# Performance work log

Measured on AMD Instinct MI355X. Metric: run time of the kernel, lower is better.

## Reference

```python
import jax, jax.numpy as jnp
import numpy as np

L, H, E, FF, MAXP, NKNOW = 4, 8, 512, 2048, 10, 1000
B, S = 4, 128
HD = E // H


def _layer_norm(x, g, b, eps=1e-5):
    m = x.mean(-1, keepdims=True)
    v = ((x - m) ** 2).mean(-1, keepdims=True)
    return (x - m) / jnp.sqrt(v + eps) * g + b


def setup_inputs() -> dict:
    key = jax.random.key(0)
    ks = jax.random.split(key, 16)
    x = jax.random.normal(ks[0], (B, S, E), jnp.float32)
    adj = jax.random.randint(ks[1], (B, S, S), 0, 2, jnp.int32)
    s_mask = jax.random.randint(ks[2], (B, S, S), 0, 2, jnp.int32)
    o_mask = jax.random.randint(ks[3], (B, S, S), 0, 2, jnp.int32)
    knowledge = jax.random.normal(ks[4], (NKNOW, E), jnp.float32)
    know_adj = jax.random.randint(ks[5], (B, S, S), 0, NKNOW, jnp.int64)
    pos_mask = jax.random.randint(ks[6], (S, S), 0, MAXP + 1, jnp.int32)
    # relative position embedding tables (padding_idx=0 -> row 0 zero)
    pe_k = jax.random.normal(ks[7], (MAXP + 1, HD), jnp.float32).at[0].set(0.0)
    pe_v = jax.random.normal(ks[8], (MAXP + 1, HD), jnp.float32).at[0].set(0.0)
    sc = 0.02
    # stacked per-layer parameters
    Wq = jax.random.normal(ks[9], (L, E, E), jnp.float32) * sc
    Wk = jax.random.normal(ks[10], (L, E, E), jnp.float32) * sc
    Wvs = jax.random.normal(ks[11], (L, E, E), jnp.float32) * sc
    Wvo = jax.random.normal(ks[12], (L, E, E), jnp.float32) * sc
    Wo = jax.random.normal(ks[13], (L, E, E), jnp.float32) * sc
    Wkn = jax.random.normal(ks[14], (L, E, E), jnp.float32) * sc
    kf = jax.random.split(ks[15], 4)
    w1 = jax.random.normal(kf[0], (L, FF, E), jnp.float32) * sc
    b1 = jnp.zeros((L, FF), jnp.float32)
    w2 = jax.random.normal(kf[1], (L, E, FF), jnp.float32) * sc
    b2 = jnp.zeros((L, E), jnp.float32)
    ln1_g = jnp.ones((L, E), jnp.float32)
    ln1_b = jnp.zeros((L, E), jnp.float32)
    ln2_g = jnp.ones((L, E), jnp.float32)
    ln2_b = jnp.zeros((L, E), jnp.float32)
    return dict(x=x, adj=adj, s_mask=s_mask, o_mask=o_mask, knowledge=knowledge,
                know_adj=know_adj, pos_mask=pos_mask, pe_k=pe_k, pe_v=pe_v,
                Wq=Wq, Wk=Wk, Wvs=Wvs, Wvo=Wvo, Wo=Wo, Wkn=Wkn,
                ln1_g=ln1_g, ln1_b=ln1_b, w1=w1, b1=b1, w2=w2, b2=b2,
                ln2_g=ln2_g, ln2_b=ln2_b)


def reference(x, adj, s_mask, o_mask, knowledge, know_adj, pos_mask, pe_k, pe_v,
              Wq, Wk, Wvs, Wvo, Wo, Wkn, ln1_g, ln1_b, w1, b1, w2, b2,
              ln2_g, ln2_b):
    bsz, slen, emb = x.shape
    hd = emb // H
    scaling = float(hd) ** (-0.5)
    # relative position embeddings, shared across batch/heads: [S,S,hd]
    pos = jnp.clip(pos_mask, 0, MAXP)
    rel_k = pe_k[pos]
    rel_v = pe_v[pos]
    adj_f = adj.astype(x.dtype)[:, None, :, :]          # [B,1,S,S]
    sm = s_mask.astype(x.dtype)[:, None, :, :, None]    # [B,1,S,S,1]
    om = o_mask.astype(x.dtype)[:, None, :, :, None]
    know_feat = knowledge[know_adj]                      # [B,S,S,E]

    def split_heads(t):  # [B,S,E] -> [B,H,S,hd]
        return t.reshape(bsz, slen, H, hd).transpose(0, 2, 1, 3)

    h = x
    for i in range(L):
        q = split_heads(h @ Wq[i].T)
        k = split_heads(h @ Wk[i].T)
        vs = split_heads(h @ Wvs[i].T)
        vo = split_heads(h @ Wvo[i].T)
        # knowledge projection -> [B,H,S,S,hd]
        know = (know_feat @ Wkn[i].T).reshape(bsz, slen, slen, H, hd).transpose(0, 3, 1, 2, 4)
        # multiplicative attention: q_i * (k_j + know_ij + rel_ij) summed over hd
        rel = (know + rel_k[None, None]) + k[:, :, None, :, :]
        scores = jnp.einsum('bhid,bhijd->bhij', q, rel) * scaling
        scores = scores - (1.0 - adj_f) * 1e30          # mask_logic
        attn = jax.nn.softmax(scores, axis=-1)           # [B,H,S,S]
        value = vs[:, :, None, :, :] * sm + vo[:, :, None, :, :] * om  # [B,H,S,S,hd]
        attn_sum = jnp.einsum('bhijd,bhij->bhid', value + rel_v[None, None], attn)
        out = attn_sum.transpose(0, 2, 1, 3).reshape(bsz, slen, emb) @ Wo[i].T
        h = _layer_norm(h + out, ln1_g[i], ln1_b[i])
        ff = jax.nn.relu(h @ w1[i].T + b1[i]) @ w2[i].T + b2[i]
        h = _layer_norm(h + ff, ln2_g[i], ln2_b[i])
    return h
```

## Files before the change

kernel.cpp:

```cpp
#include <hip/hip_runtime.h>

#define EE 512
#define SS 128
#define BB 4
#define NH 8
#define HD 64
#define FFD 2048
#define NL 4
#define LDQ 2048

typedef short bf16x8 __attribute__((ext_vector_type(8)));
typedef float f32x4 __attribute__((ext_vector_type(4)));

__device__ __forceinline__ ushort f2bf(float f) {
    uint u = __float_as_uint(f);
    return (ushort)((u + 0x7fffu + ((u >> 16) & 1u)) >> 16);
}
__device__ __forceinline__ float bflo(uint u) { return __uint_as_float(u << 16); }
__device__ __forceinline__ float bfhi(uint u) { return __uint_as_float(u & 0xffff0000u); }

__device__ __forceinline__ void gll16(const ushort* g, ushort* l) {
    __builtin_amdgcn_global_load_lds(
        (const __attribute__((address_space(1))) void*)g,
        (__attribute__((address_space(3))) void*)l, 16, 0, 0);
}

struct GemmJob {
    const ushort* A; const ushort* B;
    float* Cf; ushort* Cb;
    const float* bias; const float* resid;
    int M, N, K, flags, nbx, base;
};

__global__ __launch_bounds__(256) void gemm_bf16(GemmJob j0, GemmJob j1, int njobs)
{
    __shared__ ushort As[3][2048];
    __shared__ ushort Bs[3][4096];
    GemmJob j = (njobs > 1 && (int)blockIdx.x >= j1.base) ? j1 : j0;
    const int bid = (int)blockIdx.x - j.base;
    const int by = bid / j.nbx, bx = bid % j.nbx;
    const int rowBase = by * 32, colBase = bx * 64;
    const int t = threadIdx.x, lane = t & 63, wid = t >> 6;
    const int wc = wid;
    const int Kd = j.K, Md = j.M, Nd = j.N;

    const ushort* Bg = j.B + (size_t)(colBase + lane) * Kd;
    int gr = rowBase + (lane & 31); if (gr >= Md) gr = Md - 1;
    const ushort* Ag = j.A + (size_t)gr * Kd + (2 * wid + (lane >> 5)) * 8;

    f32x4 acc[2];
#pragma unroll
    for (int m = 0; m < 2; ++m)
#pragma unroll
        for (int r = 0; r < 4; ++r) acc[m][r] = 0.f;

    auto STAGE = [&](int bf, int tt) {
        const int k0 = tt << 6;
        gll16(Bg + k0 + (2 * wid) * 8,     &Bs[bf][(2 * wid) * 512]);
        gll16(Bg + k0 + (2 * wid + 1) * 8, &Bs[bf][(2 * wid + 1) * 512]);
        gll16(Ag + k0,                     &As[bf][(2 * wid) * 256]);
    };
    auto COMPUTE = [&](int bf) {
#pragma unroll
        for (int kc = 0; kc < 2; ++kc) {
            const int c16 = kc * 4 + (lane >> 4);
            bf16x8 af[2], bfg;
#pragma unroll
            for (int m = 0; m < 2; ++m) {
                const int row = m * 16 + (lane & 15);
                af[m] = *(const bf16x8*)&As[bf][c16 * 256 + row * 8];
            }
            {
                const int rowb = wc * 16 + (lane & 15);
                bfg = *(const bf16x8*)&Bs[bf][c16 * 512 + rowb * 8];
            }
#pragma unroll
            for (int m = 0; m < 2; ++m)
                acc[m] = __builtin_amdgcn_mfma_f32_16x16x32_bf16(af[m], bfg, acc[m], 0, 0, 0);
        }
    };

    const int nt = Kd >> 6;
    STAGE(0, 0);
    STAGE(1, 1);
    asm volatile("s_waitcnt vmcnt(3)" ::: "memory");
    __builtin_amdgcn_s_barrier();
    int bc = 0, bs = 2;
    for (int tt = 0; tt < nt; ++tt) {
        const bool more = (tt + 2) < nt;
        if (more) STAGE(bs, tt + 2);
        COMPUTE(bc);
        if (tt < nt - 1) {
            if (more) asm volatile("s_waitcnt vmcnt(3)" ::: "memory");
            else      asm volatile("s_waitcnt vmcnt(0)" ::: "memory");
            __builtin_amdgcn_s_barrier();
        }
        bc = bc == 2 ? 0 : bc + 1;
        bs = bs == 2 ? 0 : bs + 1;
    }

    const int cl = lane & 15, rh = lane >> 4;
#pragma unroll
    for (int m = 0; m < 2; ++m) {
        const int col = colBase + wc * 16 + cl;
        const int row0 = rowBase + m * 16 + rh * 4;
#pragma unroll
        for (int r = 0; r < 4; ++r) {
            const int rr = row0 + r;
            if (rr < Md) {
                float v = acc[m][r];
                if (j.flags & 1) v += j.bias[col];
                if (j.flags & 2) v = fmaxf(v, 0.f);
                if (j.resid) v += j.resid[(size_t)rr * Nd + col];
                if (j.Cf) j.Cf[(size_t)rr * Nd + col] = v;
                if (j.Cb) j.Cb[(size_t)rr * Nd + col] = f2bf(v);
            }
        }
    }
}

__global__ __launch_bounds__(256) void score_gemm(
    const ushort* __restrict__ qkvv, const ushort* __restrict__ kprojl,
    float* __restrict__ qk, float* __restrict__ qkk)
{
    __shared__ ushort As[2048];
    __shared__ ushort Bs[4096];
    const int t = threadIdx.x, lane = t & 63, wid = t >> 6;
    const int bid = blockIdx.x;
    const ushort *Abase, *Bbase;
    float* Cbase; int crs, rowBase, colBase;
    if (bid < 256) {
        const int q = bid >> 3, sub = bid & 7;
        const int b = q >> 3, h = q & 7;
        rowBase = (sub >> 1) * 32; colBase = (sub & 1) * 64;
        Abase = qkvv + (size_t)(b * SS) * LDQ + h * HD;
        Bbase = qkvv + (size_t)(b * SS) * LDQ + 512 + h * HD;
        Cbase = qk + (size_t)b * 131072 + h * 128;
        crs = 1024;
    } else {
        const int idx = bid - 256;
        const int h = idx >> 8, sub = idx & 255;
        rowBase = (sub >> 4) * 32; colBase = (sub & 15) * 64;
        Abase = qkvv + h * HD;
        Bbase = kprojl + h * HD;
        Cbase = qkk + (size_t)h * 1024;
        crs = 8192;
    }
    {
        const ushort* Bg = Bbase + (size_t)(colBase + lane) * LDQ;
        const ushort* Ag = Abase + (size_t)(rowBase + (lane & 31)) * LDQ
                           + (2 * wid + (lane >> 5)) * 8;
        gll16(Bg + (2 * wid) * 8,     &Bs[(2 * wid) * 512]);
        gll16(Bg + (2 * wid + 1) * 8, &Bs[(2 * wid + 1) * 512]);
        gll16(Ag,                     &As[(2 * wid) * 256]);
        asm volatile("s_waitcnt vmcnt(0)" ::: "memory");
        __builtin_amdgcn_s_barrier();
    }
    f32x4 acc[2];
#pragma unroll
    for (int m = 0; m < 2; ++m)
#pragma unroll
        for (int r = 0; r < 4; ++r) acc[m][r] = 0.f;
#pragma unroll
    for (int kc = 0; kc < 2; ++kc) {
        const int c16 = kc * 4 + (lane >> 4);
        bf16x8 af[2], bfg;
#pragma unroll
        for (int m = 0; m < 2; ++m) {
            const int row = m * 16 + (lane & 15);
            af[m] = *(const bf16x8*)&As[c16 * 256 + row * 8];
        }
        {
            const int rowb = wid * 16 + (lane & 15);
            bfg = *(const bf16x8*)&Bs[c16 * 512 + rowb * 8];
        }
#pragma unroll
        for (int m = 0; m < 2; ++m)
            acc[m] = __builtin_amdgcn_mfma_f32_16x16x32_bf16(af[m], bfg, acc[m], 0, 0, 0);
    }
    const int cl = lane & 15, rh = lane >> 4;
#pragma unroll
    for (int m = 0; m < 2; ++m) {
        const int col = colBase + wid * 16 + cl;
        const int row0 = rowBase + m * 16 + rh * 4;
#pragma unroll
        for (int r = 0; r < 4; ++r)
            Cbase[(size_t)(row0 + r) * crs + col] = acc[m][r];
    }
}

struct PrepArgs {
    const float *Wq, *Wk, *Wvs, *Wvo, *Wo, *Wkn, *w1, *w2, *know, *x, *pek;
    ushort *wqkvv, *wo, *wkn, *w1b, *w2b, *knowb, *hb, *kpe;
    float *h;
};
#define P4_WQKVV 1048576
#define P4_B1 (P4_WQKVV + 262144)
#define P4_B2 (P4_B1 + 262144)
#define P4_B3 (P4_B2 + 1048576)
#define P4_B4 (P4_B3 + 1048576)
#define P4_B5 (P4_B4 + 128000)
#define P4_B6 (P4_B5 + 65536)
#define P4_TOT (P4_B6 + 5632)

__global__ __launch_bounds__(256) void prep_kernel(PrepArgs pa)
{
    const int i = blockIdx.x * 256 + threadIdx.x;
    if (i >= P4_TOT) return;
    const float4* src;
    ushort4* dst;
    if (i < P4_WQKVV) {
        const int l = i >> 18, r = i & 262143, q = r >> 16;
        const float* s = (q == 0 ? pa.Wq : q == 1 ? pa.Wk : q == 2 ? pa.Wvs : pa.Wvo);
        src = (const float4*)s + l * 65536 + (r & 65535);
        dst = (ushort4*)pa.wqkvv + i;
    } else if (i < P4_B1) {
        const int k = i - P4_WQKVV;
        src = (const float4*)pa.Wo + k; dst = (ushort4*)pa.wo + k;
    } else if (i < P4_B2) {
        const int k = i - P4_B1;
        src = (const float4*)pa.Wkn + k; dst = (ushort4*)pa.wkn + k;
    } else if (i < P4_B3) {
        const int k = i - P4_B2;
        src = (const float4*)pa.w1 + k; dst = (ushort4*)pa.w1b + k;
    } else if (i < P4_B4) {
        const int k = i - P4_B3;
        src = (const float4*)pa.w2 + k; dst = (ushort4*)pa.w2b + k;
    } else if (i < P4_B5) {
        const int k = i - P4_B4;
        src = (const float4*)pa.know + k; dst = (ushort4*)pa.knowb + k;
    } else if (i < P4_B6) {
        const int k = i - P4_B5;
        src = (const float4*)pa.x + k; dst = (ushort4*)pa.hb + k;
        ((float4*)pa.h)[k] = *src;
    } else {
        const int k = i - P4_B6;
        const int c4 = k * 4;
        const int p = c4 >> 11, col = c4 & 2047, d = col & 63;
        src = (const float4*)(pa.pek + p * 64 + d);
        dst = (ushort4*)(pa.kpe + (size_t)(1000 + p) * 2048 + col);
    }
    float4 v = *src;
    ushort4 o; o.x = f2bf(v.x); o.y = f2bf(v.y); o.z = f2bf(v.z); o.w = f2bf(v.w);
    *dst = o;
}

__global__ __launch_bounds__(256) void ln_kernel(
    const float* __restrict__ X, const float* __restrict__ g,
    const float* __restrict__ bt, float* __restrict__ Yf,
    ushort* __restrict__ Yb, int rows)
{
    const int w = threadIdx.x >> 6, lane = threadIdx.x & 63;
    const int row = blockIdx.x * 4 + w;
    if (row >= rows) return;
    const float* x = X + (size_t)row * EE;
    float4 v0 = ((const float4*)x)[lane];
    float4 v1 = ((const float4*)x)[lane + 64];
    float s  = v0.x + v0.y + v0.z + v0.w + v1.x + v1.y + v1.z + v1.w;
    float q2 = v0.x*v0.x + v0.y*v0.y + v0.z*v0.z + v0.w*v0.w
             + v1.x*v1.x + v1.y*v1.y + v1.z*v1.z + v1.w*v1.w;
#pragma unroll
    for (int o = 32; o; o >>= 1) { s += __shfl_xor(s, o); q2 += __shfl_xor(q2, o); }
    const float mean = s * (1.f / EE);
    const float var  = q2 * (1.f / EE) - mean * mean;
    const float rstd = rsqrtf(var + 1e-5f);
    float4 g0 = ((const float4*)g)[lane],  g1 = ((const float4*)g)[lane + 64];
    float4 b0 = ((const float4*)bt)[lane], b1 = ((const float4*)bt)[lane + 64];
    float4 o0, o1;
    o0.x = (v0.x - mean) * rstd * g0.x + b0.x;
    o0.y = (v0.y - mean) * rstd * g0.y + b0.y;
    o0.z = (v0.z - mean) * rstd * g0.z + b0.z;
    o0.w = (v0.w - mean) * rstd * g0.w + b0.w;
    o1.x = (v1.x - mean) * rstd * g1.x + b1.x;
    o1.y = (v1.y - mean) * rstd * g1.y + b1.y;
    o1.z = (v1.z - mean) * rstd * g1.z + b1.z;
    o1.w = (v1.w - mean) * rstd * g1.w + b1.w;
    float* y = Yf + (size_t)row * EE;
    ((float4*)y)[lane] = o0;
    ((float4*)y)[lane + 64] = o1;
    ushort* yb = Yb + (size_t)row * EE;
    ushort4 p0, p1;
    p0.x = f2bf(o0.x); p0.y = f2bf(o0.y); p0.z = f2bf(o0.z); p0.w = f2bf(o0.w);
    p1.x = f2bf(o1.x); p1.y = f2bf(o1.y); p1.z = f2bf(o1.z); p1.w = f2bf(o1.w);
    ((ushort4*)yb)[lane] = p0;
    ((ushort4*)yb)[lane + 64] = p1;
}

__global__ __launch_bounds__(256) void attn_kernel(
    const ushort* __restrict__ qkvv, const float* __restrict__ qk,
    const float* __restrict__ qkk,
    const int* __restrict__ know_adj, const int* __restrict__ pos_mask,
    const float* __restrict__ pe_v,
    const int* __restrict__ adj, const int* __restrict__ s_mask,
    const int* __restrict__ o_mask, ushort* __restrict__ asum)
{
    const int blk = blockIdx.x;
    const int b = blk >> 7, i = blk & 127;
    const int t = threadIdx.x;

    __shared__ float sc[NH][SS];
    __shared__ float ap[NH][11];
    __shared__ float ws_s[SS], wo_s[SS], amask_s[SS];
    __shared__ int   pos_s[SS], n_s[SS];

    const float* qkrow  = qk + (size_t)b * 131072 + (size_t)i * 1024;
    const float* qkkrow = qkk + (size_t)(b * SS + i) * 8192;

    if (t < 128) {
        const int jj = t;
        const size_t off = ((size_t)(b * SS + i)) * SS + jj;
        n_s[jj]     = know_adj[off];
        amask_s[jj] = adj[off] ? 0.f : 1e30f;
        ws_s[jj]    = (float)s_mask[off];
        wo_s[jj]    = (float)o_mask[off];
        int p = pos_mask[i * SS + jj];
        pos_s[jj] = p > 10 ? 10 : (p < 0 ? 0 : p);
        if (t < 88) ap[t / 11][t % 11] = 0.f;
    } else {
        const int tt = t - 128;
        ((float4*)&sc[0][0])[tt]       = ((const float4*)qkrow)[tt];
        ((float4*)&sc[0][0])[tt + 128] = ((const float4*)qkrow)[tt + 128];
    }
    __syncthreads();

    {
        const int h = t >> 5, j0 = (t & 31) * 4;
        const float* qh = qkkrow + h * 1024;
#pragma unroll
        for (int u = 0; u < 4; ++u) {
            const int jj = j0 + u;
            const float v = sc[h][jj] + qh[n_s[jj]] + qh[1000 + pos_s[jj]];
            sc[h][jj] = v * 0.125f - amask_s[jj];
        }
    }
    __syncthreads();

    {
        const int w = t >> 6, lane = t & 63;
#pragma unroll
        for (int hh = 0; hh < 2; ++hh) {
            const int h = w * 2 + hh;
            float v0 = sc[h][lane], v1 = sc[h][lane + 64];
            float m = fmaxf(v0, v1);
#pragma unroll
            for (int o = 32; o; o >>= 1) m = fmaxf(m, __shfl_xor(m, o));
            float e0 = __expf(v0 - m), e1 = __expf(v1 - m);
            float ssum = e0 + e1;
#pragma unroll
            for (int o = 32; o; o >>= 1) ssum += __shfl_xor(ssum, o);
            const float inv = 1.f / ssum;
            e0 *= inv; e1 *= inv;
            sc[h][lane] = e0; sc[h][lane + 64] = e1;
            atomicAdd(&ap[h][pos_s[lane]], e0);
            atomicAdd(&ap[h][pos_s[lane + 64]], e1);
        }
    }
    __syncthreads();

    {
        const int h = t >> 5, d0 = (t & 31) * 2;
        float a0 = 0.f, a1 = 0.f;
        const ushort* vbase = qkvv + (size_t)b * SS * LDQ + 1024 + h * HD + d0;
        for (int j0 = 0; j0 < SS; j0 += 8) {
            uint vsp[8], vop[8];
#pragma unroll
            for (int u = 0; u < 8; ++u) {
                const ushort* r = vbase + (size_t)(j0 + u) * LDQ;
                vsp[u] = *(const uint*)r;
                vop[u] = *(const uint*)(r + 512);
            }
#pragma unroll
            for (int u = 0; u < 8; ++u) {
                const int jj = j0 + u;
                const float aw = sc[h][jj];
                const float wsj = ws_s[jj], woj = wo_s[jj];
                a0 += aw * (wsj * bflo(vsp[u]) + woj * bflo(vop[u]));
                a1 += aw * (wsj * bfhi(vsp[u]) + woj * bfhi(vop[u]));
            }
        }
#pragma unroll
        for (int p = 0; p < 11; ++p) {
            const float apv = ap[h][p];
            a0 += apv * pe_v[p * HD + d0];
            a1 += apv * pe_v[p * HD + d0 + 1];
        }
        const uint o = (uint)f2bf(a0) | ((uint)f2bf(a1) << 16);
        *(uint*)(asum + (size_t)(b * SS + i) * EE + h * HD + d0) = o;
    }
}

extern "C" void kernel_launch(void* const* d_in, const int* in_sizes, int n_in,
                              void* d_out, int out_size, void* d_ws, size_t ws_size,
                              hipStream_t stream)
{
    const float* x         = (const float*)d_in[0];
    const int*   adj       = (const int*)d_in[1];
    const int*   s_mask    = (const int*)d_in[2];
    const int*   o_mask    = (const int*)d_in[3];
    const float* knowledge = (const float*)d_in[4];
    const int*   know_adj  = (const int*)d_in[5];
    const int*   pos_mask  = (const int*)d_in[6];
    const float* pe_k      = (const float*)d_in[7];
    const float* pe_v      = (const float*)d_in[8];
    const float* Wq        = (const float*)d_in[9];
    const float* Wk        = (const float*)d_in[10];
    const float* Wvs       = (const float*)d_in[11];
    const float* Wvo       = (const float*)d_in[12];
    const float* Wo        = (const float*)d_in[13];
    const float* Wkn       = (const float*)d_in[14];
    const float* ln1_g     = (const float*)d_in[15];
    const float* ln1_b     = (const float*)d_in[16];
    const float* w1        = (const float*)d_in[17];
    const float* b1        = (const float*)d_in[18];
    const float* w2        = (const float*)d_in[19];
    const float* b2        = (const float*)d_in[20];
    const float* ln2_g     = (const float*)d_in[21];
    const float* ln2_b     = (const float*)d_in[22];

    const int NTOK = BB * SS;
    const size_t NTE = (size_t)NTOK * EE;

    float*  h      = (float*)d_ws;
    float*  xt     = h + NTE;
    float*  qk     = xt + NTE;
    float*  qkk    = qk + (size_t)NTOK * 1024;
    ushort* hb     = (ushort*)(qkk + (size_t)NTOK * 8192);
    ushort* qkvv   = hb + NTE;
    ushort* kprojb = qkvv + (size_t)NTOK * LDQ;
    ushort* asumb  = kprojb + (size_t)1024 * LDQ;
    ushort* ffnb   = asumb + NTE;
    ushort* wqkvv  = ffnb + (size_t)NTOK * FFD;
    ushort* wob    = wqkvv + (size_t)NL * 4 * EE * EE;
    ushort* wknb   = wob + (size_t)NL * EE * EE;
    ushort* w1b    = wknb + (size_t)NL * EE * EE;
    ushort* w2b    = w1b + (size_t)NL * FFD * EE;
    ushort* knowb  = w2b + (size_t)NL * EE * FFD;

    PrepArgs pa;
    pa.Wq = Wq; pa.Wk = Wk; pa.Wvs = Wvs; pa.Wvo = Wvo; pa.Wo = Wo; pa.Wkn = Wkn;
    pa.w1 = w1; pa.w2 = w2; pa.know = knowledge; pa.x = x; pa.pek = pe_k;
    pa.wqkvv = wqkvv; pa.wo = wob; pa.wkn = wknb; pa.w1b = w1b; pa.w2b = w2b;
    pa.knowb = knowb; pa.hb = hb; pa.h = h; pa.kpe = kprojb;
    prep_kernel<<<dim3((P4_TOT + 255) / 256), dim3(256), 0, stream>>>(pa);

    const dim3 blk(256);
    for (int l = 0; l < NL; ++l) {
        GemmJob jq{};
        jq.A = hb; jq.B = wqkvv + (size_t)l * 4 * EE * EE;
        jq.Cb = qkvv; jq.M = NTOK; jq.N = 4 * EE; jq.K = EE;
        jq.nbx = 32; jq.base = 0;
        if (l == 0) {
            GemmJob jk{};
            jk.A = knowb; jk.B = wknb;
            jk.Cb = kprojb; jk.M = 1000; jk.N = NL * EE; jk.K = EE;
            jk.nbx = 32; jk.base = 512;
            gemm_bf16<<<dim3(512 + 1024), blk, 0, stream>>>(jq, jk, 2);
        } else {
            gemm_bf16<<<dim3(512), blk, 0, stream>>>(jq, jq, 1);
        }

        score_gemm<<<dim3(2304), blk, 0, stream>>>(qkvv, kprojb + (size_t)l * EE,
                                                   qk, qkk);

        attn_kernel<<<dim3(NTOK), blk, 0, stream>>>(qkvv, qk, qkk,
                                                    know_adj, pos_mask, pe_v,
                                                    adj, s_mask, o_mask, asumb);

        GemmJob jo{};
        jo.A = asumb; jo.B = wob + (size_t)l * EE * EE;
        jo.Cf = xt; jo.resid = h; jo.M = NTOK; jo.N = EE; jo.K = EE;
        jo.nbx = 8; jo.base = 0;
        gemm_bf16<<<dim3(128), blk, 0, stream>>>(jo, jo, 1);

        ln_kernel<<<dim3(128), blk, 0, stream>>>(xt, ln1_g + l * EE, ln1_b + l * EE,
                                                 h, hb, NTOK);

        GemmJob jf1{};
        jf1.A = hb; jf1.B = w1b + (size_t)l * FFD * EE;
        jf1.Cb = ffnb; jf1.bias = b1 + (size_t)l * FFD; jf1.flags = 3;
        jf1.M = NTOK; jf1.N = FFD; jf1.K = EE; jf1.nbx = 32; jf1.base = 0;
        gemm_bf16<<<dim3(512), blk, 0, stream>>>(jf1, jf1, 1);

        GemmJob jf2{};
        jf2.A = ffnb; jf2.B = w2b + (size_t)l * EE * FFD;
        jf2.Cf = xt; jf2.bias = b2 + (size_t)l * EE; jf2.resid = h; jf2.flags = 1;
        jf2.M = NTOK; jf2.N = EE; jf2.K = FFD; jf2.nbx = 8; jf2.base = 0;
        gemm_bf16<<<dim3(128), blk, 0, stream>>>(jf2, jf2, 1);

        float* lnout = (l == NL - 1) ? (float*)d_out : h;
        ln_kernel<<<dim3(128), blk, 0, stream>>>(xt, ln2_g + l * EE, ln2_b + l * EE,
                                                 lnout, hb, NTOK);
    }
}
```

Measured before the change: 525.9 us.

## Replace scalar attention kernel with MFMA P·V kernel over transposed value layout

The QKVV GEMM epilogue now writes the Vs/Vo columns in a transposed [b,h,d,j] layout with an extra K-extension block. The rel_v positional table is preloaded into that extension by the prep kernel. A new pv_kernel computes the softmax for 16 query rows per block and does the weighted value sum as a single bf16 MFMA matmul over K=320: P·s_mask, P·o_mask and the position-bucket probabilities. This replaces the per-token scalar FMA loop. The GEMM pipeline also goes from a 3-stage to a 4-stage LDS ring. The cost is bf16 rounding of the attention probabilities and scattered uncoalesced stores in the GEMM epilogue.

```diff
diff --git a/kernel.cpp b/kernel.cpp
--- a/kernel.cpp
+++ b/kernel.cpp
@@ -8,6 +8,8 @@
 #define FFD 2048
 #define NL 4
 #define LDQ 2048
+#define KEXT 320
+#define PSTR 136
 
 typedef short bf16x8 __attribute__((ext_vector_type(8)));
 typedef float f32x4 __attribute__((ext_vector_type(4)));
@@ -27,15 +29,15 @@
 
 struct GemmJob {
     const ushort* A; const ushort* B;
-    float* Cf; ushort* Cb;
+    float* Cf; ushort* Cb; ushort* vext;
     const float* bias; const float* resid;
     int M, N, K, flags, nbx, base;
 };
 
 __global__ __launch_bounds__(256) void gemm_bf16(GemmJob j0, GemmJob j1, int njobs)
 {
-    __shared__ ushort As[3][2048];
-    __shared__ ushort Bs[3][4096];
+    __shared__ ushort As[4][2048];
+    __shared__ ushort Bs[4][4096];
     GemmJob j = (njobs > 1 && (int)blockIdx.x >= j1.base) ? j1 : j0;
     const int bid = (int)blockIdx.x - j.base;
     const int by = bid / j.nbx, bx = bid % j.nbx;
@@ -81,39 +83,41 @@
     };
 
     const int nt = Kd >> 6;
-    STAGE(0, 0);
-    STAGE(1, 1);
-    asm volatile("s_waitcnt vmcnt(3)" ::: "memory");
+    STAGE(0, 0); STAGE(1, 1); STAGE(2, 2);
+    asm volatile("s_waitcnt vmcnt(6)" ::: "memory");
     __builtin_amdgcn_s_barrier();
-    int bc = 0, bs = 2;
     for (int tt = 0; tt < nt; ++tt) {
-        const bool more = (tt + 2) < nt;
-        if (more) STAGE(bs, tt + 2);
-        COMPUTE(bc);
+        if (tt + 3 < nt) STAGE((tt + 3) & 3, tt + 3);
+        COMPUTE(tt & 3);
         if (tt < nt - 1) {
-            if (more) asm volatile("s_waitcnt vmcnt(3)" ::: "memory");
-            else      asm volatile("s_waitcnt vmcnt(0)" ::: "memory");
+            if (tt + 3 < nt)      asm volatile("s_waitcnt vmcnt(6)" ::: "memory");
+            else if (tt + 2 < nt) asm volatile("s_waitcnt vmcnt(3)" ::: "memory");
+            else                  asm volatile("s_waitcnt vmcnt(0)" ::: "memory");
             __builtin_amdgcn_s_barrier();
         }
-        bc = bc == 2 ? 0 : bc + 1;
-        bs = bs == 2 ? 0 : bs + 1;
     }
 
     const int cl = lane & 15, rh = lane >> 4;
 #pragma unroll
     for (int m = 0; m < 2; ++m) {
         const int col = colBase + wc * 16 + cl;
-        const int row0 = rowBase + m * 16 + rh * 4;
 #pragma unroll
         for (int r = 0; r < 4; ++r) {
-            const int rr = row0 + r;
+            const int rr = rowBase + m * 16 + rh * 4 + r;
             if (rr < Md) {
                 float v = acc[m][r];
                 if (j.flags & 1) v += j.bias[col];
                 if (j.flags & 2) v = fmaxf(v, 0.f);
                 if (j.resid) v += j.resid[(size_t)rr * Nd + col];
-                if (j.Cf) j.Cf[(size_t)rr * Nd + col] = v;
-                if (j.Cb) j.Cb[(size_t)rr * Nd + col] = f2bf(v);
+                if ((j.flags & 4) && col >= 1024) {
+                    const int cc = col - 1024;
+                    const int hh = (cc >> 6) & 7, d = cc & 63, vv = cc >> 9;
+                    const int bb = rr >> 7, jj2 = rr & 127;
+                    j.vext[((size_t)((bb * 8 + hh) * 64 + d)) * KEXT + vv * 128 + jj2] = f2bf(v);
+                } else {
+                    if (j.Cf) j.Cf[(size_t)rr * Nd + col] = v;
+                    if (j.Cb) j.Cb[(size_t)rr * Nd + col] = f2bf(v);
+                }
             }
         }
     }
@@ -189,9 +193,123 @@
     }
 }
 
+__global__ __launch_bounds__(256) void pv_kernel(
+    const ushort* __restrict__ vext, const float* __restrict__ qk,
+    const float* __restrict__ qkk,
+    const int* __restrict__ know_adj, const int* __restrict__ pos_mask,
+    const int* __restrict__ adj, const int* __restrict__ s_mask,
+    const int* __restrict__ o_mask, ushort* __restrict__ asum)
+{
+    __shared__ ushort Ps[40 * PSTR];
+    __shared__ ushort Bs[40 * 512];
+    __shared__ float ap[16][11];
+    const int blk = blockIdx.x;
+    const int ib = blk & 7, h = (blk >> 3) & 7, b = blk >> 6;
+    const int t = threadIdx.x, lane = t & 63, wid = t >> 6;
+
+    if (t < 176) ap[t / 11][t % 11] = 0.f;
+    __syncthreads();
+
+    {
+        const ushort* vbase = vext + ((size_t)((b * 8 + h) * 64) + lane) * KEXT;
+#pragma unroll
+        for (int s = 0; s < 5; ++s) {
+            const int c = s * 8 + wid * 2;
+            gll16(vbase + c * 8,       &Bs[c * 512]);
+            gll16(vbase + (c + 1) * 8, &Bs[(c + 1) * 512]);
+        }
+    }
+
+    {
+        const int r = t >> 4, g = t & 15;
+        const int i = ib * 16 + r;
+        const int tok = b * 128 + i;
+        const float* qkrow  = qk + (size_t)b * 131072 + (size_t)i * 1024 + h * 128 + g * 8;
+        const float* qkkrow = qkk + (size_t)tok * 8192 + h * 1024;
+        const int base = tok * 128 + g * 8;
+        const int pb   = i * 128 + g * 8;
+        int4 kn0 = *(const int4*)(know_adj + base), kn1 = *(const int4*)(know_adj + base + 4);
+        int4 ad0 = *(const int4*)(adj + base),      ad1 = *(const int4*)(adj + base + 4);
+        int4 sm0 = *(const int4*)(s_mask + base),   sm1 = *(const int4*)(s_mask + base + 4);
+        int4 om0 = *(const int4*)(o_mask + base),   om1 = *(const int4*)(o_mask + base + 4);
+        int4 po0 = *(const int4*)(pos_mask + pb),   po1 = *(const int4*)(pos_mask + pb + 4);
+        float4 q0 = *(const float4*)qkrow,          q1 = *(const float4*)(qkrow + 4);
+        int kn[8] = {kn0.x, kn0.y, kn0.z, kn0.w, kn1.x, kn1.y, kn1.z, kn1.w};
+        int ad[8] = {ad0.x, ad0.y, ad0.z, ad0.w, ad1.x, ad1.y, ad1.z, ad1.w};
+        int sm[8] = {sm0.x, sm0.y, sm0.z, sm0.w, sm1.x, sm1.y, sm1.z, sm1.w};
+        int om[8] = {om0.x, om0.y, om0.z, om0.w, om1.x, om1.y, om1.z, om1.w};
+        int po[8] = {po0.x, po0.y, po0.z, po0.w, po1.x, po1.y, po1.z, po1.w};
+        float qv[8] = {q0.x, q0.y, q0.z, q0.w, q1.x, q1.y, q1.z, q1.w};
+        float e[8];
+        int pcl[8];
+        float mx = -3e38f;
+#pragma unroll
+        for (int u = 0; u < 8; ++u) {
+            int p = po[u]; p = p < 0 ? 0 : (p > 10 ? 10 : p);
+            pcl[u] = p;
+            float sc = (qv[u] + qkkrow[kn[u]] + qkkrow[1000 + p]) * 0.125f;
+            if (!ad[u]) sc -= 1e30f;
+            e[u] = sc; mx = fmaxf(mx, sc);
+        }
+        mx = fmaxf(mx, __shfl_xor(mx, 1));
+        mx = fmaxf(mx, __shfl_xor(mx, 2));
+        mx = fmaxf(mx, __shfl_xor(mx, 4));
+        mx = fmaxf(mx, __shfl_xor(mx, 8));
+        float sum = 0.f;
+#pragma unroll
+        for (int u = 0; u < 8; ++u) { e[u] = __expf(e[u] - mx); sum += e[u]; }
+        sum += __shfl_xor(sum, 1);
+        sum += __shfl_xor(sum, 2);
+        sum += __shfl_xor(sum, 4);
+        sum += __shfl_xor(sum, 8);
+        const float inv = 1.f / sum;
+        ushort p1v[8], p2v[8];
+#pragma unroll
+        for (int u = 0; u < 8; ++u) {
+            const float a = e[u] * inv;
+            p1v[u] = f2bf(a * (float)sm[u]);
+            p2v[u] = f2bf(a * (float)om[u]);
+            atomicAdd(&ap[r][pcl[u]], a);
+        }
+        *(uint4*)&Ps[g * PSTR + r * 8]        = *(uint4*)p1v;
+        *(uint4*)&Ps[(16 + g) * PSTR + r * 8] = *(uint4*)p2v;
+    }
+    __syncthreads();
+
+#pragma unroll
+    for (int u = 0; u < 4; ++u) {
+        const int idx = t * 4 + u;
+        const int k = 256 + (idx & 63), rr = idx >> 6;
+        const float v = (k < 267) ? ap[rr][k - 256] : 0.f;
+        Ps[(k >> 3) * PSTR + rr * 8 + (k & 7)] = f2bf(v);
+    }
+    __syncthreads();
+
+    f32x4 acc;
+#pragma unroll
+    for (int r = 0; r < 4; ++r) acc[r] = 0.f;
+#pragma unroll
+    for (int s = 0; s < 5; ++s) {
+#pragma unroll
+        for (int kc = 0; kc < 2; ++kc) {
+            const int ch = s * 8 + kc * 4 + (lane >> 4);
+            bf16x8 af = *(const bf16x8*)&Ps[ch * PSTR + (lane & 15) * 8];
+            bf16x8 bfg = *(const bf16x8*)&Bs[ch * 512 + (wid * 16 + (lane & 15)) * 8];
+            acc = __builtin_amdgcn_mfma_f32_16x16x32_bf16(af, bfg, acc, 0, 0, 0);
+        }
+    }
+    const int cl = lane & 15, rh = lane >> 4;
+    const int col = wid * 16 + cl;
+#pragma unroll
+    for (int r = 0; r < 4; ++r) {
+        const int rowv = rh * 4 + r;
+        asum[(size_t)(b * 128 + ib * 16 + rowv) * 512 + h * 64 + col] = f2bf(acc[r]);
+    }
+}
+
 struct PrepArgs {
-    const float *Wq, *Wk, *Wvs, *Wvo, *Wo, *Wkn, *w1, *w2, *know, *x, *pek;
-    ushort *wqkvv, *wo, *wkn, *w1b, *w2b, *knowb, *hb, *kpe;
+    const float *Wq, *Wk, *Wvs, *Wvo, *Wo, *Wkn, *w1, *w2, *know, *x, *pek, *pev;
+    ushort *wqkvv, *wo, *wkn, *w1b, *w2b, *knowb, *hb, *kpe, *vext;
     float *h;
 };
 #define P4_WQKVV 1048576
@@ -201,12 +319,26 @@
 #define P4_B4 (P4_B3 + 1048576)
 #define P4_B5 (P4_B4 + 128000)
 #define P4_B6 (P4_B5 + 65536)
-#define P4_TOT (P4_B6 + 5632)
+#define P4_B7 (P4_B6 + 5632)
+#define P4_TOT (P4_B7 + 32768)
 
 __global__ __launch_bounds__(256) void prep_kernel(PrepArgs pa)
 {
     const int i = blockIdx.x * 256 + threadIdx.x;
     if (i >= P4_TOT) return;
+    if (i >= P4_B7) {
+        const int k = i - P4_B7;
+        const int bh = k >> 10, r2 = k & 1023, d = r2 >> 4, s4 = r2 & 15;
+        ushort o[4];
+#pragma unroll
+        for (int c = 0; c < 4; ++c) {
+            const int p = s4 * 4 + c;
+            o[c] = (p < 11) ? f2bf(pa.pev[p * 64 + d]) : (ushort)0;
+        }
+        *(ushort4*)(pa.vext + ((size_t)(bh * 64 + d)) * KEXT + 256 + s4 * 4)
+            = *(ushort4*)o;
+        return;
+    }
     const float4* src;
     ushort4* dst;
     if (i < P4_WQKVV) {
@@ -286,109 +418,6 @@
     ((ushort4*)yb)[lane + 64] = p1;
 }
 
-__global__ __launch_bounds__(256) void attn_kernel(
-    const ushort* __restrict__ qkvv, const float* __restrict__ qk,
-    const float* __restrict__ qkk,
-    const int* __restrict__ know_adj, const int* __restrict__ pos_mask,
-    const float* __restrict__ pe_v,
-    const int* __restrict__ adj, const int* __restrict__ s_mask,
-    const int* __restrict__ o_mask, ushort* __restrict__ asum)
-{
-    const int blk = blockIdx.x;
-    const int b = blk >> 7, i = blk & 127;
-    const int t = threadIdx.x;
-
-    __shared__ float sc[NH][SS];
-    __shared__ float ap[NH][11];
-    __shared__ float ws_s[SS], wo_s[SS], amask_s[SS];
-    __shared__ int   pos_s[SS], n_s[SS];
-
-    const float* qkrow  = qk + (size_t)b * 131072 + (size_t)i * 1024;
-    const float* qkkrow = qkk + (size_t)(b * SS + i) * 8192;
-
-    if (t < 128) {
-        const int jj = t;
-        const size_t off = ((size_t)(b * SS + i)) * SS + jj;
-        n_s[jj]     = know_adj[off];
-        amask_s[jj] = adj[off] ? 0.f : 1e30f;
-        ws_s[jj]    = (float)s_mask[off];
-        wo_s[jj]    = (float)o_mask[off];
-        int p = pos_mask[i * SS + jj];
-        pos_s[jj] = p > 10 ? 10 : (p < 0 ? 0 : p);
-        if (t < 88) ap[t / 11][t % 11] = 0.f;
-    } else {
-        const int tt = t - 128;
-        ((float4*)&sc[0][0])[tt]       = ((const float4*)qkrow)[tt];
-        ((float4*)&sc[0][0])[tt + 128] = ((const float4*)qkrow)[tt + 128];
-    }
-    __syncthreads();
-
-    {
-        const int h = t >> 5, j0 = (t & 31) * 4;
-        const float* qh = qkkrow + h * 1024;
-#pragma unroll
-        for (int u = 0; u < 4; ++u) {
-            const int jj = j0 + u;
-            const float v = sc[h][jj] + qh[n_s[jj]] + qh[1000 + pos_s[jj]];
-            sc[h][jj] = v * 0.125f - amask_s[jj];
-        }
-    }
-    __syncthreads();
-
-    {
-        const int w = t >> 6, lane = t & 63;
-#pragma unroll
-        for (int hh = 0; hh < 2; ++hh) {
-            const int h = w * 2 + hh;
-            float v0 = sc[h][lane], v1 = sc[h][lane + 64];
-            float m = fmaxf(v0, v1);
-#pragma unroll
-            for (int o = 32; o; o >>= 1) m = fmaxf(m, __shfl_xor(m, o));
-            float e0 = __expf(v0 - m), e1 = __expf(v1 - m);
-            float ssum = e0 + e1;
-#pragma unroll
-            for (int o = 32; o; o >>= 1) ssum += __shfl_xor(ssum, o);
-            const float inv = 1.f / ssum;
-            e0 *= inv; e1 *= inv;
-            sc[h][lane] = e0; sc[h][lane + 64] = e1;
-            atomicAdd(&ap[h][pos_s[lane]], e0);
-            atomicAdd(&ap[h][pos_s[lane + 64]], e1);
-        }
-    }
-    __syncthreads();
-
-    {
-        const int h = t >> 5, d0 = (t & 31) * 2;
-        float a0 = 0.f, a1 = 0.f;
-        const ushort* vbase = qkvv + (size_t)b * SS * LDQ + 1024 + h * HD + d0;
-        for (int j0 = 0; j0 < SS; j0 += 8) {
-            uint vsp[8], vop[8];
-#pragma unroll
-            for (int u = 0; u < 8; ++u) {
-                const ushort* r = vbase + (size_t)(j0 + u) * LDQ;
-                vsp[u] = *(const uint*)r;
-                vop[u] = *(const uint*)(r + 512);
-            }
-#pragma unroll
-            for (int u = 0; u < 8; ++u) {
-                const int jj = j0 + u;
-                const float aw = sc[h][jj];
-                const float wsj = ws_s[jj], woj = wo_s[jj];
-                a0 += aw * (wsj * bflo(vsp[u]) + woj * bflo(vop[u]));
-                a1 += aw * (wsj * bfhi(vsp[u]) + woj * bfhi(vop[u]));
-            }
-        }
-#pragma unroll
-        for (int p = 0; p < 11; ++p) {
-            const float apv = ap[h][p];
-            a0 += apv * pe_v[p * HD + d0];
-            a1 += apv * pe_v[p * HD + d0 + 1];
-        }
-        const uint o = (uint)f2bf(a0) | ((uint)f2bf(a1) << 16);
-        *(uint*)(asum + (size_t)(b * SS + i) * EE + h * HD + d0) = o;
-    }
-}
-
 extern "C" void kernel_launch(void* const* d_in, const int* in_sizes, int n_in,
                               void* d_out, int out_size, void* d_ws, size_t ws_size,
                               hipStream_t stream)
@@ -435,19 +464,21 @@
     ushort* w1b    = wknb + (size_t)NL * EE * EE;
     ushort* w2b    = w1b + (size_t)NL * FFD * EE;
     ushort* knowb  = w2b + (size_t)NL * EE * FFD;
+    ushort* vextb  = knowb + (size_t)1000 * EE;
 
     PrepArgs pa;
     pa.Wq = Wq; pa.Wk = Wk; pa.Wvs = Wvs; pa.Wvo = Wvo; pa.Wo = Wo; pa.Wkn = Wkn;
-    pa.w1 = w1; pa.w2 = w2; pa.know = knowledge; pa.x = x; pa.pek = pe_k;
+    pa.w1 = w1; pa.w2 = w2; pa.know = knowledge; pa.x = x; pa.pek = pe_k; pa.pev = pe_v;
     pa.wqkvv = wqkvv; pa.wo = wob; pa.wkn = wknb; pa.w1b = w1b; pa.w2b = w2b;
-    pa.knowb = knowb; pa.hb = hb; pa.h = h; pa.kpe = kprojb;
+    pa.knowb = knowb; pa.hb = hb; pa.h = h; pa.kpe = kprojb; pa.vext = vextb;
     prep_kernel<<<dim3((P4_TOT + 255) / 256), dim3(256), 0, stream>>>(pa);
 
     const dim3 blk(256);
     for (int l = 0; l < NL; ++l) {
         GemmJob jq{};
         jq.A = hb; jq.B = wqkvv + (size_t)l * 4 * EE * EE;
-        jq.Cb = qkvv; jq.M = NTOK; jq.N = 4 * EE; jq.K = EE;
+        jq.Cb = qkvv; jq.vext = vextb; jq.flags = 4;
+        jq.M = NTOK; jq.N = 4 * EE; jq.K = EE;
         jq.nbx = 32; jq.base = 0;
         if (l == 0) {
             GemmJob jk{};
@@ -462,9 +493,8 @@
         score_gemm<<<dim3(2304), blk, 0, stream>>>(qkvv, kprojb + (size_t)l * EE,
                                                    qk, qkk);
 
-        attn_kernel<<<dim3(NTOK), blk, 0, stream>>>(qkvv, qk, qkk,
-                                                    know_adj, pos_mask, pe_v,
-                                                    adj, s_mask, o_mask, asumb);
+        pv_kernel<<<dim3(256), blk, 0, stream>>>(vextb, qk, qkk, know_adj, pos_mask,
+                                                 adj, s_mask, o_mask, asumb);
 
         GemmJob jo{};
         jo.A = asumb; jo.B = wob + (size_t)l * EE * EE;
```

New measurement: 503.8 us. 4.2% less time.
